# Kernel optimization log

Hardware: AMD Instinct MI355X
Metric: run time of the kernel (lower is better)

Reference implementation:

```python
import jax, jax.numpy as jnp
import numpy as np

UNITS = 400    # LSTM cells per hidden layer
KATT = 10     # attention Gaussians
NCHARS = 73   # alphabet size
NMIX = 20     # bivariate GMM components


def _peephole_step(x, h, c, Wx, Wh, b, p):
    # p: [3, U] peephole weights (i, f, o)
    z = x @ Wx + h @ Wh + b                       # [B, 4U]
    zi, zf, zg, zo = jnp.split(z, 4, axis=-1)
    i = jax.nn.sigmoid(zi + p[0] * c)
    f = jax.nn.sigmoid(zf + p[1] * c)
    c_new = f * c + i * jnp.tanh(zg)
    o = jax.nn.sigmoid(zo + p[2] * c_new)
    return o * jnp.tanh(c_new), c_new


def _forward(input_strokes, char_onehot, char_mask,
             Wx0, Wh0, b0, p0, Wx1, Wh1, b1, p1, Wx2, Wh2, b2, p2,
             W_att, b_att, W_mdn, b_mdn):
    B, T, _ = input_strokes.shape
    Uc = char_onehot.shape[1]
    dt = input_strokes.dtype
    u = jnp.arange(Uc, dtype=dt)                  # character positions

    def step(carry, x_t):
        h1, c1, h2, c2, h3, c3, kappa, w = carry
        # layer 1: [stroke, window]
        h1, c1 = _peephole_step(jnp.concatenate([x_t, w], -1), h1, c1, Wx0, Wh0, b0, p0)
        # Graves soft-window attention from h1
        att = h1 @ W_att + b_att                  # [B, 3K]
        a_hat, b_hat, k_hat = jnp.split(att, 3, axis=-1)
        alpha = jnp.exp(a_hat)
        beta = jnp.exp(b_hat)
        kappa = kappa + jnp.exp(k_hat)            # [B, K] monotone position
        diff = kappa[:, :, None] - u[None, None, :]                   # [B, K, Uc]
        phi = jnp.sum(alpha[:, :, None] * jnp.exp(-beta[:, :, None] * diff * diff), axis=1)
        phi = phi * char_mask                     # [B, Uc] mask padded chars
        w = jnp.einsum('bu,buc->bc', phi, char_onehot)                # [B, NCHARS]
        # layers 2/3 with skip connections
        h2, c2 = _peephole_step(jnp.concatenate([x_t, w, h1], -1), h2, c2, Wx1, Wh1, b1, p1)
        h3, c3 = _peephole_step(jnp.concatenate([x_t, w, h2], -1), h3, c3, Wx2, Wh2, b2, p2)
        return (h1, c1, h2, c2, h3, c3, kappa, w), h3

    zh = jnp.zeros((B, UNITS), dt)
    carry0 = (zh, zh, zh, zh, zh, zh,
              jnp.zeros((B, KATT), dt), jnp.zeros((B, NCHARS), dt))
    _, hs = jax.lax.scan(step, carry0, input_strokes.transpose(1, 0, 2))
    outputs = hs.transpose(1, 0, 2)               # [B, T, UNITS]

    # mixture density head: 6*M + 1 outputs
    y = outputs @ W_mdn + b_mdn                   # [B, T, 6M+1]
    M = NMIX
    pi, mu1, mu2, s1, s2, rho, eos = jnp.split(
        y, [M, 2 * M, 3 * M, 4 * M, 5 * M, 6 * M], axis=-1)
    return jnp.concatenate([
        jax.nn.softmax(pi, axis=-1), mu1, mu2,
        jnp.exp(s1), jnp.exp(s2), jnp.tanh(rho), jax.nn.sigmoid(eos)], axis=-1)


def setup_inputs() -> dict:
    key = jax.random.key(0)
    ks = jax.random.split(key, 16)
    B, T, Uc = 32, 400, 50
    s = 0.1
    in0 = 3 + NCHARS                 # stroke + window
    in12 = 3 + NCHARS + UNITS        # stroke + window + skip h
    d = {
        'input_strokes': jax.random.normal(ks[0], (B, T, 3), jnp.float32),
        'input_chars': jax.random.randint(ks[1], (B, Uc), 0, NCHARS),
        'input_char_lens': jax.random.randint(ks[2], (B,), 10, Uc + 1),
        'Wx0': s * jax.random.normal(ks[3], (in0, 4 * UNITS), jnp.float32),
        'Wh0': s * jax.random.normal(ks[4], (UNITS, 4 * UNITS), jnp.float32),
        'b0': jnp.zeros((4 * UNITS,), jnp.float32),
        'p0': s * jax.random.normal(ks[5], (3, UNITS), jnp.float32),
        'Wx1': s * jax.random.normal(ks[6], (in12, 4 * UNITS), jnp.float32),
        'Wh1': s * jax.random.normal(ks[7], (UNITS, 4 * UNITS), jnp.float32),
        'b1': jnp.zeros((4 * UNITS,), jnp.float32),
        'p1': s * jax.random.normal(ks[8], (3, UNITS), jnp.float32),
        'Wx2': s * jax.random.normal(ks[9], (in12, 4 * UNITS), jnp.float32),
        'Wh2': s * jax.random.normal(ks[10], (UNITS, 4 * UNITS), jnp.float32),
        'b2': jnp.zeros((4 * UNITS,), jnp.float32),
        'p2': s * jax.random.normal(ks[11], (3, UNITS), jnp.float32),
        'W_att': s * jax.random.normal(ks[12], (UNITS, 3 * KATT), jnp.float32),
        'b_att': jnp.zeros((3 * KATT,), jnp.float32),
        'W_mdn': s * jax.random.normal(ks[13], (UNITS, 6 * NMIX + 1), jnp.float32),
        'b_mdn': jnp.zeros((6 * NMIX + 1,), jnp.float32),
    }
    return d


def reference(input_strokes, input_chars, input_char_lens,
              Wx0, Wh0, b0, p0, Wx1, Wh1, b1, p1, Wx2, Wh2, b2, p2,
              W_att, b_att, W_mdn, b_mdn):
    char_onehot = jax.nn.one_hot(input_chars, NCHARS, dtype=input_strokes.dtype)
    Uc = input_chars.shape[1]
    char_mask = (jnp.arange(Uc)[None, :] < input_char_lens[:, None]).astype(input_strokes.dtype)
    return _forward(input_strokes, char_onehot, char_mask,
                    Wx0, Wh0, b0, p0, Wx1, Wh1, b1, p1, Wx2, Wh2, b2, p2,
                    W_att, b_att, W_mdn, b_mdn)
```

## Files before the change

kernel.cpp:

```cpp
#include <hip/hip_runtime.h>


#define NATT   8
#define NBLK   208
#define NTHR   1024
#define TSTEPS 400
#define BATCH  32
#define UNITSN 400
#define NCHARS 73
#define UC     50
#define KTOT   2228
#define WSTR   2236
#define NGRP   8
#define NFLAG  32

typedef unsigned int       u32;
typedef unsigned long long u64;

#define STATE_BYTES 4096
#define HSLOT     12832
#define H1_BYTE   4096
#define H2_BYTE   (H1_BYTE + TSTEPS * HSLOT * 4)
#define H3_BYTE   (H2_BYTE + TSTEPS * HSLOT * 4)
#define WSLOT     2368
#define WH_BYTE   (H3_BYTE + TSTEPS * HSLOT * 4)

__device__ __forceinline__ float sigf(float x)   { return 1.0f / (1.0f + __expf(-x)); }
__device__ __forceinline__ float tanhf_(float x) { return 1.0f - 2.0f / (1.0f + __expf(2.0f * x)); }

__device__ __forceinline__ float dot100(const float* __restrict__ w,
                                        const float* __restrict__ x) {
  const float4* wv = (const float4*)w;
  const float4* xv = (const float4*)x;
  float s0 = 0.f, s1 = 0.f, s2 = 0.f, s3 = 0.f;
#pragma unroll 5
  for (int i = 0; i < 25; ++i) {
    float4 a = wv[i], bb = xv[i];
    s0 = fmaf(a.x, bb.x, s0); s1 = fmaf(a.y, bb.y, s1);
    s2 = fmaf(a.z, bb.z, s2); s3 = fmaf(a.w, bb.w, s3);
  }
  return (s0 + s1) + (s2 + s3);
}

__device__ __forceinline__ void dot100x2(const float* __restrict__ wa,
                                         const float* __restrict__ wb,
                                         const float* __restrict__ x,
                                         float& ra, float& rb) {
  const float4* av = (const float4*)wa;
  const float4* bv = (const float4*)wb;
  const float4* xv = (const float4*)x;
  float a0 = 0.f, a1 = 0.f, a2 = 0.f, a3 = 0.f;
  float c0 = 0.f, c1 = 0.f, c2 = 0.f, c3 = 0.f;
#pragma unroll 5
  for (int i = 0; i < 25; ++i) {
    float4 xx = xv[i], aa = av[i], bb = bv[i];
    a0 = fmaf(aa.x, xx.x, a0); a1 = fmaf(aa.y, xx.y, a1);
    a2 = fmaf(aa.z, xx.z, a2); a3 = fmaf(aa.w, xx.w, a3);
    c0 = fmaf(bb.x, xx.x, c0); c1 = fmaf(bb.y, xx.y, c1);
    c2 = fmaf(bb.z, xx.z, c2); c3 = fmaf(bb.w, xx.w, c3);
  }
  ra += (a0 + a1) + (a2 + a3);
  rb += (c0 + c1) + (c2 + c3);
}

__device__ __forceinline__ void dotP3(const float* __restrict__ wA,
                                      const float* __restrict__ wB,
                                      const float* __restrict__ x2,
                                      const float* __restrict__ wC,
                                      const float* __restrict__ wD,
                                      const float* __restrict__ x1,
                                      const float* __restrict__ wE,
                                      const float* __restrict__ x3,
                                      float& r3, float& r2, float& r1) {
  const float4* Av = (const float4*)wA;
  const float4* Bv = (const float4*)wB;
  const float4* Cv = (const float4*)wC;
  const float4* Dv = (const float4*)wD;
  const float4* Ev = (const float4*)wE;
  const float4* x2v = (const float4*)x2;
  const float4* x1v = (const float4*)x1;
  const float4* x3v = (const float4*)x3;
  float sA0 = 0.f, sA1 = 0.f, sA2 = 0.f, sA3 = 0.f;
  float sB0 = 0.f, sB1 = 0.f, sB2 = 0.f, sB3 = 0.f;
  float sC0 = 0.f, sC1 = 0.f, sC2 = 0.f, sC3 = 0.f;
  float sD0 = 0.f, sD1 = 0.f, sD2 = 0.f, sD3 = 0.f;
  float sE0 = 0.f, sE1 = 0.f, sE2 = 0.f, sE3 = 0.f;
#pragma unroll 2
  for (int i = 0; i < 25; ++i) {
    float4 xa = x2v[i], xb = x1v[i], xc = x3v[i];
    float4 a = Av[i], bb = Bv[i], cc = Cv[i], d = Dv[i], e = Ev[i];
    sA0 = fmaf(a.x, xa.x, sA0);  sA1 = fmaf(a.y, xa.y, sA1);
    sA2 = fmaf(a.z, xa.z, sA2);  sA3 = fmaf(a.w, xa.w, sA3);
    sB0 = fmaf(bb.x, xa.x, sB0); sB1 = fmaf(bb.y, xa.y, sB1);
    sB2 = fmaf(bb.z, xa.z, sB2); sB3 = fmaf(bb.w, xa.w, sB3);
    sC0 = fmaf(cc.x, xb.x, sC0); sC1 = fmaf(cc.y, xb.y, sC1);
    sC2 = fmaf(cc.z, xb.z, sC2); sC3 = fmaf(cc.w, xb.w, sC3);
    sD0 = fmaf(d.x, xb.x, sD0);  sD1 = fmaf(d.y, xb.y, sD1);
    sD2 = fmaf(d.z, xb.z, sD2);  sD3 = fmaf(d.w, xb.w, sD3);
    sE0 = fmaf(e.x, xc.x, sE0);  sE1 = fmaf(e.y, xc.y, sE1);
    sE2 = fmaf(e.z, xc.z, sE2);  sE3 = fmaf(e.w, xc.w, sE3);
  }
  r3 += (sA0 + sA1) + (sA2 + sA3) + (sE0 + sE1) + (sE2 + sE3);
  r2 += (sB0 + sB1) + (sB2 + sB3) + (sC0 + sC1) + (sC2 + sC3);
  r1 += (sD0 + sD1) + (sD2 + sD3);
}

__device__ __forceinline__ void dot73x3(const float* __restrict__ w1,
                                        const float* __restrict__ w2,
                                        const float* __restrict__ w3,
                                        const float* __restrict__ x, int kq,
                                        float& r1, float& r2, float& r3) {
  int st = (kq == 0) ? 0 : 18 * kq + 1;
  int en = st + ((kq == 0) ? 19 : 18);
  float s1 = 0.f, s2 = 0.f, s3 = 0.f;
  for (int k = st; k < en; ++k) {
    float xv = x[k];
    s1 = fmaf(w1[k], xv, s1); s2 = fmaf(w2[k], xv, s2); s3 = fmaf(w3[k], xv, s3);
  }
  r1 += s1; r2 += s2; r3 += s3;
}

extern "C" __global__ void __launch_bounds__(NTHR)
__attribute__((amdgpu_waves_per_eu(4, 4)))
hand_kernel(const float* __restrict__ xs, const int* __restrict__ chars,
            const int* __restrict__ lens,
            const float* __restrict__ Wx0, const float* __restrict__ Wh0,
            const float* __restrict__ b0, const float* __restrict__ p0,
            const float* __restrict__ Wx1, const float* __restrict__ Wh1,
            const float* __restrict__ b1, const float* __restrict__ p1,
            const float* __restrict__ Wx2, const float* __restrict__ Wh2,
            const float* __restrict__ b2, const float* __restrict__ p2,
            const float* __restrict__ Watt, const float* __restrict__ batt,
            const float* __restrict__ Wmdn, const float* __restrict__ bmdn,
            float* __restrict__ dout, char* __restrict__ wsb) {
  const int blk = blockIdx.x;
  const int tid = threadIdx.x;
  const bool is_att = (blk < NATT);

  __shared__ __align__(16) float wlw[8 * WSTR];
  __shared__ float zpart[NTHR], zpartB[NTHR];
  __shared__ float zbuf[256], zbufB[256];
  __shared__ float biasL[3][8];
  __shared__ float peepL[3][3][2];
  __shared__ float cstate[3][64];
  __shared__ int   bar_target;
  __shared__ float alphaL[40], betaL[40], kappaL[40];
  __shared__ float wlds[4 * NCHARS];
  __shared__ __align__(16) float wstg[BATCH * NCHARS + 12];

  int*   bar_i = (int*)wsb;
  int*   wcnt  = bar_i + 192;
  float* h1h   = (float*)(wsb + H1_BYTE);
  float* h2h   = (float*)(wsb + H2_BYTE);
  float* h3h   = (float*)(wsb + H3_BYTE);
  float* whh   = (float*)(wsb + WH_BYTE);

  const int out = tid & 255;
  const int b   = out >> 3;
  const int c   = out & 7;
  const int kq  = tid >> 8;
  const int u0  = 2 * (blk - NATT);

  if (tid == 0) bar_target = 0;
  if (tid < 192) cstate[tid / 64][tid % 64] = 0.f;
  if (tid < 40) kappaL[tid] = 0.f;

  if (!is_att) {
    for (int idx = tid; idx < 8 * KTOT; idx += NTHR) {
      int cc = idx / KTOT, k = idx - cc * KTOT;
      int gcol = (cc & 3) * UNITSN + u0 + (cc >> 2);
      float v;
      if (k < 476)        v = (k < 76)  ? Wx0[(size_t)k * 1600 + gcol]
                                        : Wh0[(size_t)(k - 76) * 1600 + gcol];
      else if (k < 1352) { int q = k - 476;
                          v = (q < 476) ? Wx1[(size_t)q * 1600 + gcol]
                                        : Wh1[(size_t)(q - 476) * 1600 + gcol]; }
      else               { int q = k - 1352;
                          v = (q < 476) ? Wx2[(size_t)q * 1600 + gcol]
                                        : Wh2[(size_t)(q - 476) * 1600 + gcol]; }
      wlw[cc * WSTR + k] = v;
    }
    if (tid < 24) {
      int l = tid >> 3, cc = tid & 7;
      const float* bs = (l == 0) ? b0 : (l == 1) ? b1 : b2;
      biasL[l][cc] = bs[(cc & 3) * UNITSN + u0 + (cc >> 2)];
    }
    if (tid < 18) {
      int l = tid / 6, r = (tid % 6) >> 1, ul = tid & 1;
      const float* ps = (l == 0) ? p0 : (l == 1) ? p1 : p2;
      peepL[l][r][ul] = ps[r * UNITSN + u0 + ul];
    }
  } else {
    for (int i = tid; i < 12000; i += NTHR) wlw[i] = Watt[i];
  }
  __syncthreads();

  const float* Wc   = wlw + c * WSTR;
  float*       attp = wlw + 12000;

  auto gridbar = [&]() {
    __syncthreads();
    if (tid == 0) {
      int e = ++bar_target;
      int g = blk & (NGRP - 1);
      int gsz = ((NBLK - 1 - g) >> 3) + 1;
      int a = __hip_atomic_fetch_add(bar_i + g * 16, 1, __ATOMIC_RELAXED, __HIP_MEMORY_SCOPE_AGENT);
      if (a + 1 == e * gsz) {
        int q = __hip_atomic_fetch_add(bar_i + 128, 1, __ATOMIC_RELAXED, __HIP_MEMORY_SCOPE_AGENT);
        if (((q + 1) & (NGRP - 1)) == 0) {
          for (int f = 0; f < NFLAG; ++f)
            __hip_atomic_store(bar_i + 256 + f * 16, e, __ATOMIC_RELAXED, __HIP_MEMORY_SCOPE_AGENT);
        }
      }
      int* myflag = bar_i + 256 + (blk & (NFLAG - 1)) * 16;
      while (__hip_atomic_load(myflag, __ATOMIC_RELAXED, __HIP_MEMORY_SCOPE_AGENT) < e)
        __builtin_amdgcn_s_sleep(2);
    }
    __syncthreads();
  };

  auto gates = [&](int layer, const float* zb, int bb, float* hdst) {
    union { float f[2]; u64 v; } pk;
#pragma unroll
    for (int ul = 0; ul < 2; ++ul) {
      float zi = zb[bb * 8 + ul * 4 + 0], zf = zb[bb * 8 + ul * 4 + 1];
      float zg = zb[bb * 8 + ul * 4 + 2], zo = zb[bb * 8 + ul * 4 + 3];
      float cold = cstate[layer][ul * 32 + bb];
      float ig = sigf(zi + peepL[layer][0][ul] * cold);
      float fg = sigf(zf + peepL[layer][1][ul] * cold);
      float cn = fg * cold + ig * tanhf_(zg);
      float og = sigf(zo + peepL[layer][2][ul] * cn);
      cstate[layer][ul * 32 + bb] = cn;
      pk.f[ul] = og * tanhf_(cn);
    }
    __hip_atomic_store((u64*)(hdst + bb * UNITSN + u0), pk.v,
                       __ATOMIC_RELAXED, __HIP_MEMORY_SCOPE_AGENT);
  };

  auto finalize1 = [&](int layer, float acc, float* hdst) {
    zpart[tid] = acc;
    __syncthreads();
    if (tid < 256)
      zbuf[tid] = zpart[tid] + zpart[tid + 256] + zpart[tid + 512] + zpart[tid + 768]
                + biasL[layer][tid & 7];
    __syncthreads();
    if (tid < 256 && (tid & 7) == 0) gates(layer, zbuf, tid >> 3, hdst);
  };

  auto finalizeQ = [&](float a2v, float* h2dst, float a1v, float* h1dst, bool do1) {
    zpart[tid]  = a2v;
    zpartB[tid] = a1v;
    __syncthreads();
    if (tid < 256) {
      zbuf[tid]  = zpart[tid]  + zpart[tid + 256]  + zpart[tid + 512]  + zpart[tid + 768]
                 + biasL[1][tid & 7];
      zbufB[tid] = zpartB[tid] + zpartB[tid + 256] + zpartB[tid + 512] + zpartB[tid + 768]
                 + biasL[0][tid & 7];
    }
    __syncthreads();
    if (tid < 256 && (tid & 7) == 0) {
      gates(1, zbuf, tid >> 3, h2dst);
      if (do1) gates(0, zbufB, tid >> 3, h1dst);
    }
  };

  const int bs0 = blk * 4;
  auto attention = [&](int t) {
    const float* h1g = h1h + (size_t)t * HSLOT;
    float* wdst = whh + (size_t)t * WSLOT + bs0 * NCHARS;
    for (int i = tid; i < 4 * NCHARS; i += NTHR) wlds[i] = 0.f;
    if (tid < 240) {
      int ks = tid / 30, r = tid - ks * 30;
      int bb2 = r / 15, jj2 = r - bb2 * 15;
      int j0 = 2 * jj2, j1 = j0 + 1;
      const float* h0 = h1g + (bs0 + 2 * bb2) * UNITSN + ks * 50;
      const float* h1p = h0 + UNITSN;
      const float* wv = wlw + (ks * 50) * 30;
      float s00 = 0.f, s01 = 0.f, s10 = 0.f, s11 = 0.f;
      for (int k = 0; k < 50; ++k) {
        float wa = wv[k * 30 + j0], wb = wv[k * 30 + j1];
        float ha = h0[k], hb = h1p[k];
        s00 = fmaf(ha, wa, s00); s01 = fmaf(ha, wb, s01);
        s10 = fmaf(hb, wa, s10); s11 = fmaf(hb, wb, s11);
      }
      int b0i = 2 * bb2;
      attp[(b0i * 30 + j0) * 8 + ks] = s00;
      attp[(b0i * 30 + j1) * 8 + ks] = s01;
      attp[((b0i + 1) * 30 + j0) * 8 + ks] = s10;
      attp[((b0i + 1) * 30 + j1) * 8 + ks] = s11;
    }
    __syncthreads();
    if (tid < 40) {
      int bl = tid / 10, j = tid - bl * 10;
      float ah = batt[j], bh = batt[10 + j], kh = batt[20 + j];
#pragma unroll
      for (int s = 0; s < 8; ++s) {
        ah += attp[(bl * 30 + j) * 8 + s];
        bh += attp[(bl * 30 + 10 + j) * 8 + s];
        kh += attp[(bl * 30 + 20 + j) * 8 + s];
      }
      float kap = kappaL[tid] + __expf(kh);
      kappaL[tid] = kap;
      alphaL[tid] = __expf(ah);
      betaL[tid]  = __expf(bh);
    }
    __syncthreads();
    if (tid < 4 * UC) {
      int bl = tid / UC, u = tid - bl * UC;
      if (u < lens[bs0 + bl]) {
        float ph = 0.f;
#pragma unroll
        for (int j = 0; j < 10; ++j) {
          float d = kappaL[bl * 10 + j] - (float)u;
          ph = fmaf(alphaL[bl * 10 + j], __expf(-betaL[bl * 10 + j] * d * d), ph);
        }
        atomicAdd(&wlds[bl * NCHARS + chars[(bs0 + bl) * UC + u]], ph);
      }
    }
    __syncthreads();
    for (int i = tid; i < (4 * NCHARS) / 2; i += NTHR) {
      union { float f[2]; u64 v; } pk;
      pk.f[0] = wlds[2 * i]; pk.f[1] = wlds[2 * i + 1];
      __hip_atomic_store((u64*)(wdst + 2 * i), pk.v,
                         __ATOMIC_RELAXED, __HIP_MEMORY_SCOPE_AGENT);
    }
    __syncthreads();
    if (tid == 0)
      __hip_atomic_fetch_add(wcnt, 1, __ATOMIC_RELAXED, __HIP_MEMORY_SCOPE_AGENT);
  };

  if (!is_att) {
    float acc = 0.f;
    if (kq == 0) {
      const float* xr = xs + (size_t)b * TSTEPS * 3;
      acc = Wc[0] * xr[0] + Wc[1] * xr[1] + Wc[2] * xr[2];
    }
    finalize1(0, acc, h1h);
  }
  gridbar();

  float acc_z1 = 0.f, acc_z2 = 0.f, acc_z3 = 0.f;
  for (int t = 0; t < TSTEPS; ++t) {
    if (is_att) {
      attention(t);
      gridbar();
      continue;
    }
    const float* h1t  = h1h + (size_t)t * HSLOT + b * UNITSN;
    const float* h2p  = h2h + (size_t)(t > 0 ? t - 1 : 0) * HSLOT + b * UNITSN;
    const float* h3pp = h3h + (size_t)(t > 1 ? t - 2 : 0) * HSLOT + b * UNITSN;
    const int o = kq * 100;
    float a3f = acc_z3, a2 = 0.f, a1 = 0.f;
    if (t >= 2) {
      dotP3(Wc + 1428 + o, Wc + 952 + o, h2p + o,
            Wc + 552 + o,  Wc + 76 + o,  h1t + o,
            Wc + 1828 + o, h3pp + o, a3f, a2, a1);
    } else if (t == 1) {
      dot100x2(Wc + 1428 + o, Wc + 952 + o, h2p + o, a3f, a2);
      dot100x2(Wc + 552 + o, Wc + 76 + o, h1t + o, a2, a1);
    } else {
      dot100x2(Wc + 552 + o, Wc + 76 + o, h1t + o, a2, a1);
    }
    if (kq == 0) {
      const float* xr = xs + ((size_t)b * TSTEPS + t) * 3;
      a2 += Wc[476] * xr[0] + Wc[477] * xr[1] + Wc[478] * xr[2];
      if (t < TSTEPS - 1)
        a1 += Wc[0] * xr[3] + Wc[1] * xr[4] + Wc[2] * xr[5];
    }
    if (t > 0) finalize1(2, a3f, h3h + (size_t)(t - 1) * HSLOT);
    if (tid == 0) {
      int tgt = NATT * (t + 1);
      while (__hip_atomic_load(wcnt, __ATOMIC_RELAXED, __HIP_MEMORY_SCOPE_AGENT) < tgt)
        __builtin_amdgcn_s_sleep(2);
    }
    __syncthreads();
    {
      const float4* wsrc = (const float4*)(whh + (size_t)t * WSLOT);
      for (int i = tid; i < (BATCH * NCHARS) / 4; i += NTHR)
        ((float4*)wstg)[i] = wsrc[i];
    }
    __syncthreads();
    bool do1 = (t < TSTEPS - 1);
    float q2 = a2, q1 = a1, z3n = 0.f;
    dot73x3(Wc + 479, Wc + 3, Wc + 1355, wstg + b * NCHARS, kq, q2, q1, z3n);
    if (kq == 0) {
      const float* xr = xs + ((size_t)b * TSTEPS + t) * 3;
      z3n += Wc[1352] * xr[0] + Wc[1353] * xr[1] + Wc[1354] * xr[2];
    }
    finalizeQ(q2, h2h + (size_t)t * HSLOT,
              q1, h1h + (size_t)(t + 1) * HSLOT, do1);
    acc_z3 = z3n;
    gridbar();
  }
  if (!is_att) {
    const float* h2l  = h2h + (size_t)(TSTEPS - 1) * HSLOT + b * UNITSN;
    const float* h3ll = h3h + (size_t)(TSTEPS - 2) * HSLOT + b * UNITSN;
    float a3 = acc_z3 + dot100(Wc + 1428 + kq * 100, h2l + kq * 100)
                      + dot100(Wc + 1828 + kq * 100, h3ll + kq * 100);
    finalize1(2, a3, h3h + (size_t)(TSTEPS - 1) * HSLOT);
  }
  gridbar();

  {
    int j = tid & 127, ks = tid >> 7;
    for (int i0 = 0; i0 < 64; i0 += 4) {
      float acc[4] = {0.f, 0.f, 0.f, 0.f};
      const float* hp[4];
      bool val[4];
      for (int r = 0; r < 4; ++r) {
        int row = blk + (i0 + r) * NBLK;
        val[r] = (row < 12800);
        hp[r] = val[r] ? (h3h + (size_t)(row % TSTEPS) * HSLOT + (row / TSTEPS) * UNITSN + ks * 50)
                       : h3h;
      }
      if (j < 121) {
        const float* wp = Wmdn + (size_t)(ks * 50) * 121 + j;
        for (int k = 0; k < 50; ++k) {
          float wv = wp[(size_t)k * 121];
#pragma unroll
          for (int r = 0; r < 4; ++r) acc[r] = fmaf(hp[r][k], wv, acc[r]);
        }
      }
      for (int r = 0; r < 4; ++r) {
        zpart[tid] = acc[r];
        __syncthreads();
        if (tid < 121) {
          float s = bmdn[tid];
#pragma unroll
          for (int m = 0; m < 8; ++m) s += zpart[tid + m * 128];
          zbuf[tid] = s;
        }
        __syncthreads();
        if (tid == 0) {
          float mx = zbuf[0];
          for (int q = 1; q < 20; ++q) mx = fmaxf(mx, zbuf[q]);
          float s = 0.f;
          for (int q = 0; q < 20; ++q) s += __expf(zbuf[q] - mx);
          zbuf[126] = mx;
          zbuf[127] = 1.f / s;
        }
        __syncthreads();
        if (val[r] && tid < 121) {
          int row = blk + (i0 + r) * NBLK;
          float y = zbuf[tid], o;
          if (tid < 20)       o = __expf(y - zbuf[126]) * zbuf[127];
          else if (tid < 60)  o = y;
          else if (tid < 100) o = __expf(y);
          else if (tid < 120) o = tanhf_(y);
          else                o = sigf(y);
          dout[(size_t)row * 121 + tid] = o;
        }
        __syncthreads();
      }
    }
  }
}

extern "C" void kernel_launch(void* const* d_in, const int* in_sizes, int n_in,
                              void* d_out, int out_size, void* d_ws, size_t ws_size,
                              hipStream_t stream) {
  const float* xs   = (const float*)d_in[0];
  const int*   chrs = (const int*)d_in[1];
  const int*   lens = (const int*)d_in[2];
  const float* Wx0  = (const float*)d_in[3];
  const float* Wh0  = (const float*)d_in[4];
  const float* b0   = (const float*)d_in[5];
  const float* p0   = (const float*)d_in[6];
  const float* Wx1  = (const float*)d_in[7];
  const float* Wh1  = (const float*)d_in[8];
  const float* b1   = (const float*)d_in[9];
  const float* p1   = (const float*)d_in[10];
  const float* Wx2  = (const float*)d_in[11];
  const float* Wh2  = (const float*)d_in[12];
  const float* b2   = (const float*)d_in[13];
  const float* p2   = (const float*)d_in[14];
  const float* Watt = (const float*)d_in[15];
  const float* batt = (const float*)d_in[16];
  const float* Wmdn = (const float*)d_in[17];
  const float* bmdn = (const float*)d_in[18];

  hipMemsetAsync(d_ws, 0, STATE_BYTES, stream);
  hipLaunchKernelGGL(hand_kernel, dim3(NBLK), dim3(NTHR), 0, stream,
                     xs, chrs, lens, Wx0, Wh0, b0, p0, Wx1, Wh1, b1, p1,
                     Wx2, Wh2, b2, p2, Watt, batt, Wmdn, bmdn,
                     (float*)d_out, (char*)d_ws);
}
```

Baseline: 7.286 ms.

## Merge layer-3 finalize into combined three-layer reduction and prefetch dot inputs

Removes the separate layer-3 finalize, with its two block-wide barriers per timestep, and folds its reduction and gate evaluation into one combined three-layer finalize after the attention wait. This cuts barrier count on the serial recurrent path but moves layer-3 gating later, after the window wait. It also software-pipelines the hidden-state vector loads in the fused dot product two iterations ahead, with unroll 5, to hide global load latency. This raises register pressure under the fixed waves-per-EU constraint.

New measurement: 7.523 ms. 1.03x slower.

```diff
diff --git a/kernel.cpp b/kernel.cpp
--- a/kernel.cpp
+++ b/kernel.cpp
@@ -85,9 +85,14 @@
   float sC0 = 0.f, sC1 = 0.f, sC2 = 0.f, sC3 = 0.f;
   float sD0 = 0.f, sD1 = 0.f, sD2 = 0.f, sD3 = 0.f;
   float sE0 = 0.f, sE1 = 0.f, sE2 = 0.f, sE3 = 0.f;
-#pragma unroll 2
+  float4 xa0 = x2v[0], xb0 = x1v[0], xc0 = x3v[0];
+  float4 xa1 = x2v[1], xb1 = x1v[1], xc1 = x3v[1];
+#pragma unroll 5
   for (int i = 0; i < 25; ++i) {
-    float4 xa = x2v[i], xb = x1v[i], xc = x3v[i];
+    int ip = i + 2; ip = (ip < 25) ? ip : 24;
+    float4 xa = xa0, xb = xb0, xc = xc0;
+    xa0 = xa1; xb0 = xb1; xc0 = xc1;
+    xa1 = x2v[ip]; xb1 = x1v[ip]; xc1 = x3v[ip];
     float4 a = Av[i], bb = Bv[i], cc = Cv[i], d = Dv[i], e = Ev[i];
     sA0 = fmaf(a.x, xa.x, sA0);  sA1 = fmaf(a.y, xa.y, sA1);
     sA2 = fmaf(a.z, xa.z, sA2);  sA3 = fmaf(a.w, xa.w, sA3);
@@ -138,8 +143,8 @@
   const bool is_att = (blk < NATT);
 
   __shared__ __align__(16) float wlw[8 * WSTR];
-  __shared__ float zpart[NTHR], zpartB[NTHR];
-  __shared__ float zbuf[256], zbufB[256];
+  __shared__ float zpart[NTHR], zpartB[NTHR], zpartC[NTHR];
+  __shared__ float zbuf[256], zbufB[256], zbufC[256];
   __shared__ float biasL[3][8];
   __shared__ float peepL[3][3][2];
   __shared__ float cstate[3][64];
@@ -247,20 +252,24 @@
     if (tid < 256 && (tid & 7) == 0) gates(layer, zbuf, tid >> 3, hdst);
   };
 
-  auto finalizeQ = [&](float a2v, float* h2dst, float a1v, float* h1dst, bool do1) {
-    zpart[tid]  = a2v;
-    zpartB[tid] = a1v;
+  auto finalize3 = [&](float a3v, float* h3dst, bool do3,
+                       float a2v, float* h2dst,
+                       float a1v, float* h1dst, bool do1) {
+    zpart[tid] = a3v; zpartB[tid] = a2v; zpartC[tid] = a1v;
     __syncthreads();
     if (tid < 256) {
       zbuf[tid]  = zpart[tid]  + zpart[tid + 256]  + zpart[tid + 512]  + zpart[tid + 768]
+                 + biasL[2][tid & 7];
+      zbufB[tid] = zpartB[tid] + zpartB[tid + 256] + zpartB[tid + 512] + zpartB[tid + 768]
                  + biasL[1][tid & 7];
-      zbufB[tid] = zpartB[tid] + zpartB[tid + 256] + zpartB[tid + 512] + zpartB[tid + 768]
+      zbufC[tid] = zpartC[tid] + zpartC[tid + 256] + zpartC[tid + 512] + zpartC[tid + 768]
                  + biasL[0][tid & 7];
     }
     __syncthreads();
     if (tid < 256 && (tid & 7) == 0) {
-      gates(1, zbuf, tid >> 3, h2dst);
-      if (do1) gates(0, zbufB, tid >> 3, h1dst);
+      if (do3) gates(2, zbuf, tid >> 3, h3dst);
+      gates(1, zbufB, tid >> 3, h2dst);
+      if (do1) gates(0, zbufC, tid >> 3, h1dst);
     }
   };
 
@@ -339,7 +348,7 @@
   }
   gridbar();
 
-  float acc_z1 = 0.f, acc_z2 = 0.f, acc_z3 = 0.f;
+  float acc_z3 = 0.f;
   for (int t = 0; t < TSTEPS; ++t) {
     if (is_att) {
       attention(t);
@@ -367,7 +376,6 @@
       if (t < TSTEPS - 1)
         a1 += Wc[0] * xr[3] + Wc[1] * xr[4] + Wc[2] * xr[5];
     }
-    if (t > 0) finalize1(2, a3f, h3h + (size_t)(t - 1) * HSLOT);
     if (tid == 0) {
       int tgt = NATT * (t + 1);
       while (__hip_atomic_load(wcnt, __ATOMIC_RELAXED, __HIP_MEMORY_SCOPE_AGENT) < tgt)
@@ -387,8 +395,9 @@
       const float* xr = xs + ((size_t)b * TSTEPS + t) * 3;
       z3n += Wc[1352] * xr[0] + Wc[1353] * xr[1] + Wc[1354] * xr[2];
     }
-    finalizeQ(q2, h2h + (size_t)t * HSLOT,
-              q1, h1h + (size_t)(t + 1) * HSLOT, do1);
+    finalize3(a3f, h3h + (size_t)(t > 0 ? t - 1 : 0) * HSLOT, t > 0,
+              q2,  h2h + (size_t)t * HSLOT,
+              q1,  h1h + (size_t)(t + 1) * HSLOT, do1);
     acc_z3 = z3n;
     gridbar();
   }
```

## Remove attention blocks from grid barrier; have them poll the global counter

Applied to the files above, without the earlier changes.

The 8 attention blocks stop joining the grid barrier. Only the 200 compute blocks arrive, split into equal groups. Attention blocks instead spin on the global group counter until the epoch they need, so the barrier's fan-in shrinks and compute blocks no longer wait for attention blocks to arrive. The attention h1·W_att loop is also changed to load h in float2 pairs. The cost is a separate polling path that must stay consistent with the epoch count, including the final epoch wait before the MDN phase.

After: 7.138 ms. -2.0%, faster.

```diff
diff --git a/kernel.cpp b/kernel.cpp
--- a/kernel.cpp
+++ b/kernel.cpp
@@ -3,6 +3,7 @@
 
 #define NATT   8
 #define NBLK   208
+#define NBLKC  200
 #define NTHR   1024
 #define TSTEPS 400
 #define BATCH  32
@@ -13,6 +14,7 @@
 #define WSTR   2236
 #define NGRP   8
 #define NFLAG  32
+#define NEPOCH 402
 
 typedef unsigned int       u32;
 typedef unsigned long long u64;
@@ -136,6 +138,7 @@
   const int blk = blockIdx.x;
   const int tid = threadIdx.x;
   const bool is_att = (blk < NATT);
+  const int cblk = blk - NATT;
 
   __shared__ __align__(16) float wlw[8 * WSTR];
   __shared__ float zpart[NTHR], zpartB[NTHR];
@@ -149,6 +152,7 @@
   __shared__ __align__(16) float wstg[BATCH * NCHARS + 12];
 
   int*   bar_i = (int*)wsb;
+  int*   glob  = bar_i + 128;
   int*   wcnt  = bar_i + 192;
   float* h1h   = (float*)(wsb + H1_BYTE);
   float* h2h   = (float*)(wsb + H2_BYTE);
@@ -159,7 +163,7 @@
   const int b   = out >> 3;
   const int c   = out & 7;
   const int kq  = tid >> 8;
-  const int u0  = 2 * (blk - NATT);
+  const int u0  = 2 * cblk;
 
   if (tid == 0) bar_target = 0;
   if (tid < 192) cstate[tid / 64][tid % 64] = 0.f;
@@ -202,18 +206,27 @@
     __syncthreads();
     if (tid == 0) {
       int e = ++bar_target;
-      int g = blk & (NGRP - 1);
-      int gsz = ((NBLK - 1 - g) >> 3) + 1;
+      int g = cblk & (NGRP - 1);
+      const int gsz = NBLKC / NGRP;
       int a = __hip_atomic_fetch_add(bar_i + g * 16, 1, __ATOMIC_RELAXED, __HIP_MEMORY_SCOPE_AGENT);
       if (a + 1 == e * gsz) {
-        int q = __hip_atomic_fetch_add(bar_i + 128, 1, __ATOMIC_RELAXED, __HIP_MEMORY_SCOPE_AGENT);
+        int q = __hip_atomic_fetch_add(glob, 1, __ATOMIC_RELAXED, __HIP_MEMORY_SCOPE_AGENT);
         if (((q + 1) & (NGRP - 1)) == 0) {
           for (int f = 0; f < NFLAG; ++f)
             __hip_atomic_store(bar_i + 256 + f * 16, e, __ATOMIC_RELAXED, __HIP_MEMORY_SCOPE_AGENT);
         }
       }
-      int* myflag = bar_i + 256 + (blk & (NFLAG - 1)) * 16;
+      int* myflag = bar_i + 256 + (cblk & (NFLAG - 1)) * 16;
       while (__hip_atomic_load(myflag, __ATOMIC_RELAXED, __HIP_MEMORY_SCOPE_AGENT) < e)
+        __builtin_amdgcn_s_sleep(2);
+    }
+    __syncthreads();
+  };
+
+  auto waitglob = [&](int e) {
+    if (tid == 0) {
+      int tgt = NGRP * e;
+      while (__hip_atomic_load(glob, __ATOMIC_RELAXED, __HIP_MEMORY_SCOPE_AGENT) < tgt)
         __builtin_amdgcn_s_sleep(2);
     }
     __syncthreads();
@@ -264,142 +277,146 @@
     }
   };
 
-  const int bs0 = blk * 4;
-  auto attention = [&](int t) {
-    const float* h1g = h1h + (size_t)t * HSLOT;
-    float* wdst = whh + (size_t)t * WSLOT + bs0 * NCHARS;
-    for (int i = tid; i < 4 * NCHARS; i += NTHR) wlds[i] = 0.f;
-    if (tid < 240) {
-      int ks = tid / 30, r = tid - ks * 30;
-      int bb2 = r / 15, jj2 = r - bb2 * 15;
-      int j0 = 2 * jj2, j1 = j0 + 1;
-      const float* h0 = h1g + (bs0 + 2 * bb2) * UNITSN + ks * 50;
-      const float* h1p = h0 + UNITSN;
-      const float* wv = wlw + (ks * 50) * 30;
-      float s00 = 0.f, s01 = 0.f, s10 = 0.f, s11 = 0.f;
-      for (int k = 0; k < 50; ++k) {
-        float wa = wv[k * 30 + j0], wb = wv[k * 30 + j1];
-        float ha = h0[k], hb = h1p[k];
-        s00 = fmaf(ha, wa, s00); s01 = fmaf(ha, wb, s01);
-        s10 = fmaf(hb, wa, s10); s11 = fmaf(hb, wb, s11);
-      }
-      int b0i = 2 * bb2;
-      attp[(b0i * 30 + j0) * 8 + ks] = s00;
-      attp[(b0i * 30 + j1) * 8 + ks] = s01;
-      attp[((b0i + 1) * 30 + j0) * 8 + ks] = s10;
-      attp[((b0i + 1) * 30 + j1) * 8 + ks] = s11;
-    }
-    __syncthreads();
-    if (tid < 40) {
-      int bl = tid / 10, j = tid - bl * 10;
-      float ah = batt[j], bh = batt[10 + j], kh = batt[20 + j];
+  if (is_att) {
+    const int bs0 = blk * 4;
+    for (int t = 0; t < TSTEPS; ++t) {
+      waitglob(t + 1);
+      const float* h1g = h1h + (size_t)t * HSLOT;
+      float* wdst = whh + (size_t)t * WSLOT + bs0 * NCHARS;
+      for (int i = tid; i < 4 * NCHARS; i += NTHR) wlds[i] = 0.f;
+      if (tid < 240) {
+        int ks = tid / 30, r = tid - ks * 30;
+        int bb2 = r / 15, jj2 = r - bb2 * 15;
+        int j0 = 2 * jj2, j1 = j0 + 1;
+        const float2* h0v = (const float2*)(h1g + (bs0 + 2 * bb2) * UNITSN + ks * 50);
+        const float2* h1v = (const float2*)(h1g + (bs0 + 2 * bb2 + 1) * UNITSN + ks * 50);
+        const float* wv = wlw + (ks * 50) * 30;
+        float s00 = 0.f, s01 = 0.f, s10 = 0.f, s11 = 0.f;
 #pragma unroll
-      for (int s = 0; s < 8; ++s) {
-        ah += attp[(bl * 30 + j) * 8 + s];
-        bh += attp[(bl * 30 + 10 + j) * 8 + s];
-        kh += attp[(bl * 30 + 20 + j) * 8 + s];
-      }
-      float kap = kappaL[tid] + __expf(kh);
-      kappaL[tid] = kap;
-      alphaL[tid] = __expf(ah);
-      betaL[tid]  = __expf(bh);
-    }
-    __syncthreads();
-    if (tid < 4 * UC) {
-      int bl = tid / UC, u = tid - bl * UC;
-      if (u < lens[bs0 + bl]) {
-        float ph = 0.f;
+        for (int kk = 0; kk < 25; ++kk) {
+          float2 ha = h0v[kk], hb = h1v[kk];
+          float wa0 = wv[(2 * kk) * 30 + j0],     wb0 = wv[(2 * kk) * 30 + j1];
+          float wa1 = wv[(2 * kk + 1) * 30 + j0], wb1 = wv[(2 * kk + 1) * 30 + j1];
+          s00 = fmaf(ha.x, wa0, s00); s01 = fmaf(ha.x, wb0, s01);
+          s10 = fmaf(hb.x, wa0, s10); s11 = fmaf(hb.x, wb0, s11);
+          s00 = fmaf(ha.y, wa1, s00); s01 = fmaf(ha.y, wb1, s01);
+          s10 = fmaf(hb.y, wa1, s10); s11 = fmaf(hb.y, wb1, s11);
+        }
+        int b0i = 2 * bb2;
+        attp[(b0i * 30 + j0) * 8 + ks] = s00;
+        attp[(b0i * 30 + j1) * 8 + ks] = s01;
+        attp[((b0i + 1) * 30 + j0) * 8 + ks] = s10;
+        attp[((b0i + 1) * 30 + j1) * 8 + ks] = s11;
+      }
+      __syncthreads();
+      if (tid < 40) {
+        int bl = tid / 10, j = tid - bl * 10;
+        float ah = batt[j], bh = batt[10 + j], kh = batt[20 + j];
 #pragma unroll
-        for (int j = 0; j < 10; ++j) {
-          float d = kappaL[bl * 10 + j] - (float)u;
-          ph = fmaf(alphaL[bl * 10 + j], __expf(-betaL[bl * 10 + j] * d * d), ph);
-        }
-        atomicAdd(&wlds[bl * NCHARS + chars[(bs0 + bl) * UC + u]], ph);
-      }
-    }
-    __syncthreads();
-    for (int i = tid; i < (4 * NCHARS) / 2; i += NTHR) {
-      union { float f[2]; u64 v; } pk;
-      pk.f[0] = wlds[2 * i]; pk.f[1] = wlds[2 * i + 1];
-      __hip_atomic_store((u64*)(wdst + 2 * i), pk.v,
-                         __ATOMIC_RELAXED, __HIP_MEMORY_SCOPE_AGENT);
-    }
-    __syncthreads();
-    if (tid == 0)
-      __hip_atomic_fetch_add(wcnt, 1, __ATOMIC_RELAXED, __HIP_MEMORY_SCOPE_AGENT);
-  };
-
-  if (!is_att) {
-    float acc = 0.f;
-    if (kq == 0) {
-      const float* xr = xs + (size_t)b * TSTEPS * 3;
-      acc = Wc[0] * xr[0] + Wc[1] * xr[1] + Wc[2] * xr[2];
-    }
-    finalize1(0, acc, h1h);
-  }
-  gridbar();
-
-  float acc_z1 = 0.f, acc_z2 = 0.f, acc_z3 = 0.f;
-  for (int t = 0; t < TSTEPS; ++t) {
-    if (is_att) {
-      attention(t);
+        for (int s = 0; s < 8; ++s) {
+          ah += attp[(bl * 30 + j) * 8 + s];
+          bh += attp[(bl * 30 + 10 + j) * 8 + s];
+          kh += attp[(bl * 30 + 20 + j) * 8 + s];
+        }
+        float kap = kappaL[tid] + __expf(kh);
+        kappaL[tid] = kap;
+        alphaL[tid] = __expf(ah);
+        betaL[tid]  = __expf(bh);
+      }
+      __syncthreads();
+      if (tid < 4 * UC) {
+        int bl = tid / UC, u = tid - bl * UC;
+        if (u < lens[bs0 + bl]) {
+          float ph = 0.f;
+#pragma unroll
+          for (int j = 0; j < 10; ++j) {
+            float d = kappaL[bl * 10 + j] - (float)u;
+            ph = fmaf(alphaL[bl * 10 + j], __expf(-betaL[bl * 10 + j] * d * d), ph);
+          }
+          atomicAdd(&wlds[bl * NCHARS + chars[(bs0 + bl) * UC + u]], ph);
+        }
+      }
+      __syncthreads();
+      for (int i = tid; i < (4 * NCHARS) / 2; i += NTHR) {
+        union { float f[2]; u64 v; } pk;
+        pk.f[0] = wlds[2 * i]; pk.f[1] = wlds[2 * i + 1];
+        __hip_atomic_store((u64*)(wdst + 2 * i), pk.v,
+                           __ATOMIC_RELAXED, __HIP_MEMORY_SCOPE_AGENT);
+      }
+      __syncthreads();
+      if (tid == 0)
+        __hip_atomic_fetch_add(wcnt, 1, __ATOMIC_RELAXED, __HIP_MEMORY_SCOPE_AGENT);
+    }
+    waitglob(NEPOCH);
+  }
+  else {
+    {
+      float acc = 0.f;
+      if (kq == 0) {
+        const float* xr = xs + (size_t)b * TSTEPS * 3;
+        acc = Wc[0] * xr[0] + Wc[1] * xr[1] + Wc[2] * xr[2];
+      }
+      finalize1(0, acc, h1h);
+    }
+    gridbar();
+
+    float acc_z3 = 0.f;
+    for (int t = 0; t < TSTEPS; ++t) {
+      const float* h1t  = h1h + (size_t)t * HSLOT + b * UNITSN;
+      const float* h2p  = h2h + (size_t)(t > 0 ? t - 1 : 0) * HSLOT + b * UNITSN;
+      const float* h3pp = h3h + (size_t)(t > 1 ? t - 2 : 0) * HSLOT + b * UNITSN;
+      const int o = kq * 100;
+      float a3f = acc_z3, a2 = 0.f, a1 = 0.f;
+      if (t >= 2) {
+        dotP3(Wc + 1428 + o, Wc + 952 + o, h2p + o,
+              Wc + 552 + o,  Wc + 76 + o,  h1t + o,
+              Wc + 1828 + o, h3pp + o, a3f, a2, a1);
+      } else if (t == 1) {
+        dot100x2(Wc + 1428 + o, Wc + 952 + o, h2p + o, a3f, a2);
+        dot100x2(Wc + 552 + o, Wc + 76 + o, h1t + o, a2, a1);
+      } else {
+        dot100x2(Wc + 552 + o, Wc + 76 + o, h1t + o, a2, a1);
+      }
+      if (kq == 0) {
+        const float* xr = xs + ((size_t)b * TSTEPS + t) * 3;
+        a2 += Wc[476] * xr[0] + Wc[477] * xr[1] + Wc[478] * xr[2];
+        if (t < TSTEPS - 1)
+          a1 += Wc[0] * xr[3] + Wc[1] * xr[4] + Wc[2] * xr[5];
+      }
+      if (t > 0) finalize1(2, a3f, h3h + (size_t)(t - 1) * HSLOT);
+      if (tid == 0) {
+        int tgt = NATT * (t + 1);
+        while (__hip_atomic_load(wcnt, __ATOMIC_RELAXED, __HIP_MEMORY_SCOPE_AGENT) < tgt)
+          __builtin_amdgcn_s_sleep(2);
+      }
+      __syncthreads();
+      {
+        const float4* wsrc = (const float4*)(whh + (size_t)t * WSLOT);
+        for (int i = tid; i < (BATCH * NCHARS) / 4; i += NTHR)
+          ((float4*)wstg)[i] = wsrc[i];
+      }
+      __syncthreads();
+      bool do1 = (t < TSTEPS - 1);
+      float q2 = a2, q1 = a1, z3n = 0.f;
+      dot73x3(Wc + 479, Wc + 3, Wc + 1355, wstg + b * NCHARS, kq, q2, q1, z3n);
+      if (kq == 0) {
+        const float* xr = xs + ((size_t)b * TSTEPS + t) * 3;
+        z3n += Wc[1352] * xr[0] + Wc[1353] * xr[1] + Wc[1354] * xr[2];
+      }
+      finalizeQ(q2, h2h + (size_t)t * HSLOT,
+                q1, h1h + (size_t)(t + 1) * HSLOT, do1);
+      acc_z3 = z3n;
       gridbar();
-      continue;
-    }
-    const float* h1t  = h1h + (size_t)t * HSLOT + b * UNITSN;
-    const float* h2p  = h2h + (size_t)(t > 0 ? t - 1 : 0) * HSLOT + b * UNITSN;
-    const float* h3pp = h3h + (size_t)(t > 1 ? t - 2 : 0) * HSLOT + b * UNITSN;
-    const int o = kq * 100;
-    float a3f = acc_z3, a2 = 0.f, a1 = 0.f;
-    if (t >= 2) {
-      dotP3(Wc + 1428 + o, Wc + 952 + o, h2p + o,
-            Wc + 552 + o,  Wc + 76 + o,  h1t + o,
-            Wc + 1828 + o, h3pp + o, a3f, a2, a1);
-    } else if (t == 1) {
-      dot100x2(Wc + 1428 + o, Wc + 952 + o, h2p + o, a3f, a2);
-      dot100x2(Wc + 552 + o, Wc + 76 + o, h1t + o, a2, a1);
-    } else {
-      dot100x2(Wc + 552 + o, Wc + 76 + o, h1t + o, a2, a1);
-    }
-    if (kq == 0) {
-      const float* xr = xs + ((size_t)b * TSTEPS + t) * 3;
-      a2 += Wc[476] * xr[0] + Wc[477] * xr[1] + Wc[478] * xr[2];
-      if (t < TSTEPS - 1)
-        a1 += Wc[0] * xr[3] + Wc[1] * xr[4] + Wc[2] * xr[5];
-    }
-    if (t > 0) finalize1(2, a3f, h3h + (size_t)(t - 1) * HSLOT);
-    if (tid == 0) {
-      int tgt = NATT * (t + 1);
-      while (__hip_atomic_load(wcnt, __ATOMIC_RELAXED, __HIP_MEMORY_SCOPE_AGENT) < tgt)
-        __builtin_amdgcn_s_sleep(2);
-    }
-    __syncthreads();
+    }
     {
-      const float4* wsrc = (const float4*)(whh + (size_t)t * WSLOT);
-      for (int i = tid; i < (BATCH * NCHARS) / 4; i += NTHR)
-        ((float4*)wstg)[i] = wsrc[i];
-    }
-    __syncthreads();
-    bool do1 = (t < TSTEPS - 1);
-    float q2 = a2, q1 = a1, z3n = 0.f;
-    dot73x3(Wc + 479, Wc + 3, Wc + 1355, wstg + b * NCHARS, kq, q2, q1, z3n);
-    if (kq == 0) {
-      const float* xr = xs + ((size_t)b * TSTEPS + t) * 3;
-      z3n += Wc[1352] * xr[0] + Wc[1353] * xr[1] + Wc[1354] * xr[2];
-    }
-    finalizeQ(q2, h2h + (size_t)t * HSLOT,
-              q1, h1h + (size_t)(t + 1) * HSLOT, do1);
-    acc_z3 = z3n;
+      const float* h2l  = h2h + (size_t)(TSTEPS - 1) * HSLOT + b * UNITSN;
+      const float* h3ll = h3h + (size_t)(TSTEPS - 2) * HSLOT + b * UNITSN;
+      float a3 = acc_z3 + dot100(Wc + 1428 + kq * 100, h2l + kq * 100)
+                        + dot100(Wc + 1828 + kq * 100, h3ll + kq * 100);
+      finalize1(2, a3, h3h + (size_t)(TSTEPS - 1) * HSLOT);
+    }
     gridbar();
   }
-  if (!is_att) {
-    const float* h2l  = h2h + (size_t)(TSTEPS - 1) * HSLOT + b * UNITSN;
-    const float* h3ll = h3h + (size_t)(TSTEPS - 2) * HSLOT + b * UNITSN;
-    float a3 = acc_z3 + dot100(Wc + 1428 + kq * 100, h2l + kq * 100)
-                      + dot100(Wc + 1828 + kq * 100, h3ll + kq * 100);
-    finalize1(2, a3, h3h + (size_t)(TSTEPS - 1) * HSLOT);
-  }
-  gridbar();
 
   {
     int j = tid & 127, ks = tid >> 7;
```
